# Optimization experiments

Measured on AMD Instinct MI355X. Metric: run time of the kernel, lower is better.

Reference implementation:

```python
import jax, jax.numpy as jnp
import numpy as np

B, N, T, D = 4, 128, 64, 768
L_ATTN, HEADS = 4, 8
M_SSM = 4
D_INNER, D_STATE, HEADDIM = 1536, 64, 64
NHEADS = D_INNER // HEADDIM  # 24
D_CONV = 4
CONV_DIM = D_INNER + 2 * D_STATE  # 1664
IN_PROJ = 2 * D_INNER + 2 * D_STATE + NHEADS  # 3224
FFN_MULT = 4


def rmsnorm(x, w, eps=1e-5):
    return x * jax.lax.rsqrt(jnp.mean(x * x, -1, keepdims=True) + eps) * w


def mha(q_in, kv_in, Wq, Wk, Wv, Wo):
    b, lq, d = q_in.shape
    lk = kv_in.shape[1]
    dh = d // HEADS
    scale = 1.0 / float(np.sqrt(dh))
    q = (q_in @ Wq).reshape(b, lq, HEADS, dh)
    k = (kv_in @ Wk).reshape(b, lk, HEADS, dh)
    v = (kv_in @ Wv).reshape(b, lk, HEADS, dh)
    scores = jnp.einsum('bqhd,bkhd->bhqk', q, k) * scale
    attn = jax.nn.softmax(scores, axis=-1)
    o = jnp.einsum('bhqk,bkhd->bqhd', attn, v).reshape(b, lq, d)
    return o @ Wo


def mamba_block(x, in_proj_w, conv_w, conv_b, dt_bias, A_log, D_skip, norm_w, out_proj_w):
    # x: (b, l, D); selective-scan (Mamba2) with scalar-per-head A, ngroups=1
    b, l, _ = x.shape
    zxbcdt = x @ in_proj_w                       # (b, l, IN_PROJ)
    z = zxbcdt[..., :D_INNER]
    xBC = zxbcdt[..., D_INNER:D_INNER + CONV_DIM]
    dt = zxbcdt[..., D_INNER + CONV_DIM:]        # (b, l, NHEADS)
    # causal depthwise conv1d, kernel D_CONV
    xp = jnp.pad(xBC, ((0, 0), (D_CONV - 1, 0), (0, 0)))
    xc = sum(conv_w[k] * xp[:, k:k + l] for k in range(D_CONV)) + conv_b
    xc = jax.nn.silu(xc)
    xs = xc[..., :D_INNER].reshape(b, l, NHEADS, HEADDIM)
    Bm = xc[..., D_INNER:D_INNER + D_STATE]      # (b, l, D_STATE)
    Cm = xc[..., D_INNER + D_STATE:]             # (b, l, D_STATE)
    dt = jax.nn.softplus(dt + dt_bias)           # (b, l, NHEADS)
    A = -jnp.exp(A_log)                          # (NHEADS,)
    h0 = jnp.zeros((b, NHEADS, HEADDIM, D_STATE), x.dtype)

    def step(h, inp):
        xt, Bt, Ct, dtt = inp                    # (b,nh,hd), (b,ds), (b,ds), (b,nh)
        dA = jnp.exp(dtt * A)                    # (b, nh)
        h = h * dA[:, :, None, None] + (dtt[:, :, None, None] * xt[..., None]) * Bt[:, None, None, :]
        y = jnp.einsum('bhps,bs->bhp', h, Ct)
        return h, y

    hT, ys = jax.lax.scan(step, h0, (xs.transpose(1, 0, 2, 3), Bm.transpose(1, 0, 2), Cm.transpose(1, 0, 2), dt.transpose(1, 0, 2)))
    y = ys.transpose(1, 0, 2, 3) + D_skip[:, None] * xs  # skip connection per head
    y = y.reshape(b, l, D_INNER)
    y = rmsnorm(y * jax.nn.silu(z), norm_w)      # gated RMSNorm
    return y @ out_proj_w, hT


def reference(precepts, actions, attn_norm1_w, Wq, Wk, Wv, Wo, attn_norm2_w, ffn_w1, ffn_b1, ffn_w2, ffn_b2, ssm_norm_w, in_proj_w, conv_w, conv_b, dt_bias, A_log, D_skip, mamba_norm_w, out_proj_w, proj_w, proj_b):
    p = precepts.reshape(B * N, T, D)
    a = actions.reshape(B * N, T, D)
    for i in range(L_ATTN):
        cross = (i + 1) % 2 == 0
        q = rmsnorm(p, attn_norm1_w[i])
        kv = a if cross else q
        p = p + mha(q, kv, Wq[i], Wk[i], Wv[i], Wo[i])
        h_ = rmsnorm(p, attn_norm2_w[i])
        p = p + (jax.nn.gelu(h_ @ ffn_w1[i] + ffn_b1[i]) @ ffn_w2[i] + ffn_b2[i])
    # (b n) t d -> (b t) n d : scan over the num_steps axis
    z = p.reshape(B, N, T, D).transpose(0, 2, 1, 3).reshape(B * T, N, D)
    h_last = None
    for m in range(M_SSM):
        out, h_last = mamba_block(rmsnorm(z, ssm_norm_w[m]), in_proj_w[m], conv_w[m], conv_b[m], dt_bias[m], A_log[m], D_skip[m], mamba_norm_w[m], out_proj_w[m])
        z = z + out
    y = z @ proj_w + proj_b
    y = y.reshape(B, T, N, D).transpose(0, 2, 1, 3)  # b n t d
    return y, h_last


def setup_inputs() -> dict:
    key = jax.random.key(0)
    ks = jax.random.split(key, 16)
    s = 0.02
    f32 = jnp.float32
    return {
        'precepts': jax.random.normal(ks[0], (B, N, T, D), f32),
        'actions': jax.random.normal(ks[1], (B, N, T, D), f32),
        'attn_norm1_w': jnp.ones((L_ATTN, D), f32),
        'Wq': s * jax.random.normal(ks[2], (L_ATTN, D, D), f32),
        'Wk': s * jax.random.normal(ks[3], (L_ATTN, D, D), f32),
        'Wv': s * jax.random.normal(ks[4], (L_ATTN, D, D), f32),
        'Wo': s * jax.random.normal(ks[5], (L_ATTN, D, D), f32),
        'attn_norm2_w': jnp.ones((L_ATTN, D), f32),
        'ffn_w1': s * jax.random.normal(ks[6], (L_ATTN, D, FFN_MULT * D), f32),
        'ffn_b1': jnp.zeros((L_ATTN, FFN_MULT * D), f32),
        'ffn_w2': s * jax.random.normal(ks[7], (L_ATTN, FFN_MULT * D, D), f32),
        'ffn_b2': jnp.zeros((L_ATTN, D), f32),
        'ssm_norm_w': jnp.ones((M_SSM, D), f32),
        'in_proj_w': s * jax.random.normal(ks[8], (M_SSM, D, IN_PROJ), f32),
        'conv_w': s * jax.random.normal(ks[9], (M_SSM, D_CONV, CONV_DIM), f32),
        'conv_b': jnp.zeros((M_SSM, CONV_DIM), f32),
        'dt_bias': jax.random.uniform(ks[10], (M_SSM, NHEADS), f32, -2.0, 0.0),
        'A_log': jnp.broadcast_to(jnp.log(jnp.arange(1, NHEADS + 1, dtype=f32)), (M_SSM, NHEADS)),
        'D_skip': jnp.ones((M_SSM, NHEADS), f32),
        'mamba_norm_w': jnp.ones((M_SSM, D_INNER), f32),
        'out_proj_w': s * jax.random.normal(ks[11], (M_SSM, D_INNER, D), f32),
        'proj_w': s * jax.random.normal(ks[12], (D, D), f32),
        'proj_b': jnp.zeros((D,), f32),
    }
```

## Files before the change

### kernel.cpp

```cpp
#include <hip/hip_runtime.h>
#include <hip/hip_bf16.h>
#include <math.h>

constexpr long TOK  = 32768;
constexpr long HALF = TOK * 768;
constexpr int FLAG_ACC = 1, FLAG_GELU = 2, FLAG_PERM = 4, FLAG_BF16 = 8;

typedef __bf16 bf16x8 __attribute__((ext_vector_type(8)));
typedef __bf16 bf16x4 __attribute__((ext_vector_type(4)));
typedef float  f32x4  __attribute__((ext_vector_type(4)));

__device__ __forceinline__ void gload_lds16(const void* g, void* l) {
    __builtin_amdgcn_global_load_lds(
        (const __attribute__((address_space(1))) void*)g,
        (__attribute__((address_space(3))) void*)l, 16, 0, 0);
}
__device__ __forceinline__ float bf2f(__hip_bfloat16 v) { return __bfloat162float(v); }

__global__ __launch_bounds__(256) void gemm_bf16(
    const __hip_bfloat16* __restrict__ A,
    const __hip_bfloat16* __restrict__ BT,
    const float* __restrict__ bias,
    void* __restrict__ Cv, int ldc,
    int M, int N, int K, int flags, int moff)
{
    __shared__ __hip_bfloat16 As[2][128 * 32];
    __shared__ __hip_bfloat16 Bs[2][128 * 32];
    const int tid = threadIdx.x;
    const int wv = tid >> 6, lane = tid & 63;
    const int nwg = gridDim.x * gridDim.y;
    const int orig = blockIdx.y * gridDim.x + blockIdx.x;
    const int q8 = nwg >> 3, r8 = nwg & 7;
    const int xcd = orig & 7, off = orig >> 3;
    const int wgid = (xcd < r8 ? xcd * (q8 + 1) : r8 * (q8 + 1) + (xcd - r8) * q8) + off;
    const int bm = (wgid / gridDim.x) * 128, bn = (wgid % gridDim.x) * 128;
    const int wr = (wv >> 1) * 64, wc = (wv & 1) * 64;
    const int lrow = lane & 15, lk = lane >> 4;
    const int ck = (lk ^ (lrow & 3) ^ ((lrow >> 2) & 3)) * 8;

    f32x4 acc[4][4];
#pragma unroll
    for (int n = 0; n < 4; n++)
#pragma unroll
        for (int m = 0; m < 4; m++) acc[n][m] = f32x4{0.f, 0.f, 0.f, 0.f};

    const int nk = K >> 5;
    auto stage = [&](int kt, int buf) {
#pragma unroll
        for (int i = 0; i < 2; i++) {
            const int lin = i * 256 + tid;
            const int row = lin >> 2;
            const int ks  = (((lin & 3) ^ (row & 3) ^ ((row >> 2) & 3)) * 8);
            const long asrc = (long)(bm + row) * K + kt * 32 + ks;
            const long bsrc = (long)(bn + row) * K + kt * 32 + ks;
            char* la = (char*)&As[buf][0] + (i * 256 + wv * 64) * 16;
            char* lb = (char*)&Bs[buf][0] + (i * 256 + wv * 64) * 16;
            gload_lds16(A + asrc, la);
            gload_lds16(BT + bsrc, lb);
        }
    };

    stage(0, 0);
    __syncthreads();
    for (int kt = 0; kt < nk; kt++) {
        const int cur = kt & 1;
        if (kt + 1 < nk) stage(kt + 1, cur ^ 1);
        bf16x8 af[4], bfr[4];
#pragma unroll
        for (int m = 0; m < 4; m++) {
            af[m]  = *(const bf16x8*)(const void*)&As[cur][(wr + m * 16 + lrow) * 32 + ck];
            bfr[m] = *(const bf16x8*)(const void*)&Bs[cur][(wc + m * 16 + lrow) * 32 + ck];
        }
#pragma unroll
        for (int n = 0; n < 4; n++)
#pragma unroll
            for (int m = 0; m < 4; m++)
                acc[n][m] = __builtin_amdgcn_mfma_f32_16x16x32_bf16(bfr[n], af[m], acc[n][m], 0, 0, 0);
        __syncthreads();
    }

    float* Cf = (float*)Cv;
    __hip_bfloat16* Cb = (__hip_bfloat16*)Cv;
#pragma unroll
    for (int n = 0; n < 4; n++) {
        const int gcb = bn + wc + n * 16 + lk * 4;
        f32x4 b4 = f32x4{0.f, 0.f, 0.f, 0.f};
        if (bias) b4 = *(const f32x4*)&bias[gcb];
#pragma unroll
        for (int m = 0; m < 4; m++) {
            const int gr = bm + wr + m * 16 + lrow;
            f32x4 v = acc[n][m] + b4;
            if (flags & FLAG_GELU) {
#pragma unroll
                for (int j = 0; j < 4; j++) {
                    const float x = v[j];
                    const float u = 1.5957691216057308f * (x + 0.044715f * x * x * x);
                    v[j] = x / (1.f + __expf(-u));
                }
            }
            if (flags & FLAG_PERM) {
                const int mg = moff + gr;
                const int b_ = mg >> 13, t_ = (mg >> 7) & 63, n_ = mg & 127;
                *(f32x4*)&Cf[(((long)(b_ * 128 + n_)) * 64 + t_) * ldc + gcb] = v;
            } else if (flags & FLAG_BF16) {
                __hip_bfloat16 o0 = __float2bfloat16(v[0]), o1 = __float2bfloat16(v[1]);
                __hip_bfloat16 o2 = __float2bfloat16(v[2]), o3 = __float2bfloat16(v[3]);
                ushort4 o = { *(ushort*)&o0, *(ushort*)&o1, *(ushort*)&o2, *(ushort*)&o3 };
                *(ushort4*)&Cb[(long)gr * ldc + gcb] = o;
            } else if (flags & FLAG_ACC) {
                float* dst = &Cf[(long)gr * ldc + gcb];
                f32x4 old = *(const f32x4*)dst;
                *(f32x4*)dst = old + v;
            } else {
                *(f32x4*)&Cf[(long)gr * ldc + gcb] = v;
            }
        }
    }
}

__global__ void convT_kernel(const float* __restrict__ W, __hip_bfloat16* __restrict__ WT,
                             int K, int N, int Npad)
{
    __shared__ float t[32][33];
    const int k0 = blockIdx.y * 32, n0 = blockIdx.x * 32;
    const int tx = threadIdx.x & 31, ty = threadIdx.x >> 5;
#pragma unroll
    for (int i = 0; i < 4; i++) {
        int k = k0 + ty + i * 8, n = n0 + tx;
        t[ty + i * 8][tx] = (k < K && n < N) ? W[(long)k * N + n] : 0.f;
    }
    __syncthreads();
#pragma unroll
    for (int i = 0; i < 4; i++) {
        int n = n0 + ty + i * 8, k = k0 + tx;
        if (n < Npad && k < K) WT[(long)n * K + k] = __float2bfloat16(t[tx][ty + i * 8]);
    }
}

__global__ void cvt_kernel(const float4* __restrict__ x, ushort4* __restrict__ y, long n4)
{
    long i = (long)blockIdx.x * 256 + threadIdx.x;
    if (i >= n4) return;
    float4 v = x[i];
    __hip_bfloat16 a = __float2bfloat16(v.x), b = __float2bfloat16(v.y);
    __hip_bfloat16 c = __float2bfloat16(v.z), d = __float2bfloat16(v.w);
    ushort4 o = { *(ushort*)&a, *(ushort*)&b, *(ushort*)&c, *(ushort*)&d };
    y[i] = o;
}

__global__ void rmsnorm_f32(const float* __restrict__ x, const float* __restrict__ w,
                            __hip_bfloat16* __restrict__ out, int D, int xs, int os, long nrows)
{
    const int wv = threadIdx.x >> 6, lane = threadIdx.x & 63;
    const long row = (long)blockIdx.x * 4 + wv;
    if (row >= nrows) return;
    const float* xr = x + row * xs;
    const int it = D >> 8;
    float ss = 0.f;
    for (int i = 0; i < it; i++) {
        const float4 v = *(const float4*)&xr[(i * 64 + lane) * 4];
        ss += v.x * v.x + v.y * v.y + v.z * v.z + v.w * v.w;
    }
    for (int o = 32; o; o >>= 1) ss += __shfl_xor(ss, o);
    const float sc = rsqrtf(ss / D + 1e-5f);
    __hip_bfloat16* orow = out + row * os;
    for (int i = 0; i < it; i++) {
        const int e = (i * 64 + lane) * 4;
        const float4 v = *(const float4*)&xr[e];
        const float4 g = *(const float4*)&w[e];
        bf16x4 o;
        o[0] = (__bf16)(v.x * sc * g.x); o[1] = (__bf16)(v.y * sc * g.y);
        o[2] = (__bf16)(v.z * sc * g.z); o[3] = (__bf16)(v.w * sc * g.w);
        *(bf16x4*)(void*)&orow[e] = o;
    }
}
__global__ void rmsnorm_b16(const __hip_bfloat16* __restrict__ x, const float* __restrict__ w,
                            __hip_bfloat16* __restrict__ out, int D, int xs, int os, long nrows)
{
    const int wv = threadIdx.x >> 6, lane = threadIdx.x & 63;
    const long row = (long)blockIdx.x * 4 + wv;
    if (row >= nrows) return;
    const __hip_bfloat16* xr = x + row * xs;
    const int it = D >> 8;
    float ss = 0.f;
    for (int i = 0; i < it; i++) {
        const bf16x4 v = *(const bf16x4*)(const void*)&xr[(i * 64 + lane) * 4];
#pragma unroll
        for (int e = 0; e < 4; e++) { const float f = (float)v[e]; ss += f * f; }
    }
    for (int o = 32; o; o >>= 1) ss += __shfl_xor(ss, o);
    const float sc = rsqrtf(ss / D + 1e-5f);
    __hip_bfloat16* orow = out + row * os;
    for (int i = 0; i < it; i++) {
        const int e = (i * 64 + lane) * 4;
        const bf16x4 v = *(const bf16x4*)(const void*)&xr[e];
        const float4 g = *(const float4*)&w[e];
        bf16x4 o;
        o[0] = (__bf16)((float)v[0] * sc * g.x); o[1] = (__bf16)((float)v[1] * sc * g.y);
        o[2] = (__bf16)((float)v[2] * sc * g.z); o[3] = (__bf16)((float)v[3] * sc * g.w);
        *(bf16x4*)(void*)&orow[e] = o;
    }
}

__global__ __launch_bounds__(256) void attn_kernel(
    const __hip_bfloat16* __restrict__ QKV, __hip_bfloat16* __restrict__ O)
{
    __shared__ __align__(16) __hip_bfloat16 Qs[3 * 64 * 32];
    __shared__ __align__(16) __hip_bfloat16 Ks[3 * 64 * 32];
    __shared__ __align__(16) __hip_bfloat16 VT[2 * 96 * 32];
    __shared__ __align__(16) __hip_bfloat16 Ps[2 * 64 * 32];
    const int tid = threadIdx.x;
    const int wid = tid >> 6, lane = tid & 63;
    const int lrow = lane & 15, lk = lane >> 4;
    const int b = blockIdx.x >> 3, h = blockIdx.x & 7;
    const long base = (long)b * 64 * 2304 + h * 96;

#pragma unroll
    for (int i = 0; i < 3; i++) {
        const int v = i * 256 + tid;
        const int r = v / 12, c8 = v - r * 12;
        const int kst = c8 >> 2, ch = c8 & 3, slot = ch ^ (r & 3);
        const bf16x8 q = *(const bf16x8*)(const void*)&QKV[base + (long)r * 2304 + c8 * 8];
        const bf16x8 k = *(const bf16x8*)(const void*)&QKV[base + (long)r * 2304 + 768 + c8 * 8];
        *(bf16x8*)(void*)&Qs[(kst * 64 + r) * 32 + slot * 8] = q;
        *(bf16x8*)(void*)&Ks[(kst * 64 + r) * 32 + slot * 8] = k;
    }
    for (int i = 0; i < 16; i++) {
        const int k = wid * 16 + i;
        const __hip_bfloat16* vrow = &QKV[base + (long)k * 2304 + 1536];
        const int sb = (k >> 3) & 3, khi = k >> 5, klo = k & 7;
        {
            const int d = lane;
            VT[(khi * 96 + d) * 32 + ((sb ^ (d & 3)) * 8) + klo] = vrow[d];
        }
        if (lane < 32) {
            const int d = 64 + lane;
            VT[(khi * 96 + d) * 32 + ((sb ^ (d & 3)) * 8) + klo] = vrow[d];
        }
    }
    __syncthreads();

    const int ck = (lk ^ (lrow & 3)) * 8;
    f32x4 s[4];
#pragma unroll
    for (int n = 0; n < 4; n++) s[n] = f32x4{0.f, 0.f, 0.f, 0.f};
#pragma unroll
    for (int kst = 0; kst < 3; kst++) {
        const bf16x8 qf = *(const bf16x8*)(const void*)&Qs[(kst * 64 + wid * 16 + lrow) * 32 + ck];
#pragma unroll
        for (int n = 0; n < 4; n++) {
            const bf16x8 kf = *(const bf16x8*)(const void*)&Ks[(kst * 64 + n * 16 + lrow) * 32 + ck];
            s[n] = __builtin_amdgcn_mfma_f32_16x16x32_bf16(qf, kf, s[n], 0, 0, 0);
        }
    }
    const float scale = 0.102062072615966f;
#pragma unroll
    for (int n = 0; n < 4; n++) s[n] *= scale;
    float inv[4];
#pragma unroll
    for (int j = 0; j < 4; j++) {
        float mx = fmaxf(fmaxf(s[0][j], s[1][j]), fmaxf(s[2][j], s[3][j]));
        mx = fmaxf(mx, __shfl_xor(mx, 1));
        mx = fmaxf(mx, __shfl_xor(mx, 2));
        mx = fmaxf(mx, __shfl_xor(mx, 4));
        mx = fmaxf(mx, __shfl_xor(mx, 8));
        float sum = 0.f;
#pragma unroll
        for (int n = 0; n < 4; n++) { s[n][j] = __expf(s[n][j] - mx); sum += s[n][j]; }
        sum += __shfl_xor(sum, 1);
        sum += __shfl_xor(sum, 2);
        sum += __shfl_xor(sum, 4);
        sum += __shfl_xor(sum, 8);
        inv[j] = 1.f / sum;
    }
#pragma unroll
    for (int n = 0; n < 4; n++) {
        const int k = n * 16 + lrow;
        const int kst = n >> 1, kc = ((n & 1) << 1) + (lrow >> 3), ke = lrow & 7;
#pragma unroll
        for (int j = 0; j < 4; j++) {
            const int q = wid * 16 + lk * 4 + j;
            Ps[(kst * 64 + q) * 32 + ((kc ^ (q & 3)) * 8) + ke] = __float2bfloat16(s[n][j] * inv[j]);
        }
    }
    __syncthreads();

    const int wq = wid >> 1, wd = wid & 1;
    f32x4 y[3][2];
#pragma unroll
    for (int mv = 0; mv < 3; mv++)
#pragma unroll
        for (int np = 0; np < 2; np++) y[mv][np] = f32x4{0.f, 0.f, 0.f, 0.f};
#pragma unroll
    for (int ks = 0; ks < 2; ks++) {
        bf16x8 vf[3], pf[2];
#pragma unroll
        for (int mv = 0; mv < 3; mv++)
            vf[mv] = *(const bf16x8*)(const void*)&VT[(ks * 96 + wd * 48 + mv * 16 + lrow) * 32 + ck];
#pragma unroll
        for (int np = 0; np < 2; np++)
            pf[np] = *(const bf16x8*)(const void*)&Ps[(ks * 64 + wq * 32 + np * 16 + lrow) * 32 + ck];
#pragma unroll
        for (int mv = 0; mv < 3; mv++)
#pragma unroll
            for (int np = 0; np < 2; np++)
                y[mv][np] = __builtin_amdgcn_mfma_f32_16x16x32_bf16(vf[mv], pf[np], y[mv][np], 0, 0, 0);
    }
#pragma unroll
    for (int mv = 0; mv < 3; mv++) {
        const int d0 = wd * 48 + mv * 16 + lk * 4;
#pragma unroll
        for (int np = 0; np < 2; np++) {
            const int q = wq * 32 + np * 16 + lrow;
            bf16x4 o;
#pragma unroll
            for (int j = 0; j < 4; j++) o[j] = (__bf16)y[mv][np][j];
            *(bf16x4*)(void*)&O[(long)(b * 64 + q) * 768 + h * 96 + d0] = o;
        }
    }
}

__global__ void transpose_kernel(const float* __restrict__ P, float* __restrict__ Z)
{
    long lin = (long)blockIdx.x * 256 + threadIdx.x;
    if (lin >= HALF) return;
    int d = (int)(lin % 768);
    long rowz = lin / 768;
    int n = rowz & 127, t = (int)((rowz >> 7) & 63), b = (int)(rowz >> 13);
    long rowp = ((long)(b * 128 + n)) * 64 + t;
    Z[lin] = P[rowp * 768 + d];
}

__global__ __launch_bounds__(256) void conv_kernel(
    const __hip_bfloat16* __restrict__ zx, const float* __restrict__ cw,
    const float* __restrict__ cb, __hip_bfloat16* __restrict__ xc,
    __hip_bfloat16* __restrict__ bcB, long rows)
{
    const long r = blockIdx.x;
    const int tid = threadIdx.x;
    if (tid >= 208) return;
    const int c0 = tid * 8;
    const int n = (int)(r & 127);
    float acc[8];
    {
        const float4 b0 = *(const float4*)&cb[c0];
        const float4 b1 = *(const float4*)&cb[c0 + 4];
        acc[0] = b0.x; acc[1] = b0.y; acc[2] = b0.z; acc[3] = b0.w;
        acc[4] = b1.x; acc[5] = b1.y; acc[6] = b1.z; acc[7] = b1.w;
    }
#pragma unroll
    for (int k = 0; k < 4; k++) {
        if (n - 3 + k < 0) continue;
        const bf16x8 xv = *(const bf16x8*)(const void*)&zx[(r - 3 + k) * 3328 + 1536 + c0];
        const float4 w0 = *(const float4*)&cw[k * 1664 + c0];
        const float4 w1 = *(const float4*)&cw[k * 1664 + c0 + 4];
        acc[0] += w0.x * (float)xv[0]; acc[1] += w0.y * (float)xv[1];
        acc[2] += w0.z * (float)xv[2]; acc[3] += w0.w * (float)xv[3];
        acc[4] += w1.x * (float)xv[4]; acc[5] += w1.y * (float)xv[5];
        acc[6] += w1.z * (float)xv[6]; acc[7] += w1.w * (float)xv[7];
    }
    bf16x8 o;
#pragma unroll
    for (int e = 0; e < 8; e++) {
        const float s = acc[e] / (1.f + __expf(-acc[e]));
        o[e] = (__bf16)s;
    }
    if (c0 < 1536) *(bf16x8*)(void*)&xc[r * 1664 + c0] = o;
    else           *(bf16x8*)(void*)&bcB[r * 128 + (c0 - 1536)] = o;
}

__global__ void dt_kernel(const __hip_bfloat16* __restrict__ zx, const float* __restrict__ bias,
                          float* __restrict__ dtf, long count)
{
    long lin = (long)blockIdx.x * 256 + threadIdx.x;
    if (lin >= count) return;
    int h = (int)(lin % 24);
    long r = lin / 24;
    float v = bf2f(zx[r * 3328 + 3200 + h]) + bias[h];
    dtf[lin] = (v > 0.f) ? v + log1pf(expf(-v)) : log1pf(expf(v));
}

__global__ __launch_bounds__(256) void ssd_kernel(
    const __hip_bfloat16* __restrict__ zx0, const float* __restrict__ dtf0,
    const __hip_bfloat16* __restrict__ bcB0, __hip_bfloat16* __restrict__ xc0,
    const float* __restrict__ Alog, const float* __restrict__ Dskip,
    float* __restrict__ hout, int bt0)
{
    __shared__ __align__(16) char SM[50688];
    __hip_bfloat16* Cl  = (__hip_bfloat16*)SM;
    __hip_bfloat16* Bl  = Cl + 8192;
    __hip_bfloat16* Ml  = (__hip_bfloat16*)SM;
    __hip_bfloat16* XTl = (__hip_bfloat16*)(SM + 32768);
    __hip_bfloat16* BTl = (__hip_bfloat16*)SM;
    float* cum = (float*)(SM + 49152);
    float* dtl = cum + 128;
    float* wl  = dtl + 128;

    const int tid = threadIdx.x;
    const int wid = tid >> 6, lane = tid & 63;
    const int lrow = lane & 15, lk = lane >> 4;
    const int btl = blockIdx.x / 24, h = blockIdx.x % 24;
    const long rowbase = (long)btl * 128;

    const __hip_bfloat16* zxp = zx0 + rowbase * 3328 + h * 64;
    const float* dtp = dtf0 + rowbase * 24;
    const __hip_bfloat16* bcp = bcB0 + rowbase * 128;
    __hip_bfloat16* xcp = xc0 + rowbase * 1664 + h * 64;

    const float A  = -expf(Alog[h]);
    const float Dh = Dskip[h];

#pragma unroll
    for (int i = 0; i < 4; i++) {
        const int v = tid + i * 256;
        const int row = v >> 3, c8 = v & 7;
        const int kst = c8 >> 2, ch = c8 & 3;
        const int slot = ch ^ (row & 3);
        bf16x8 vB = *(const bf16x8*)(const void*)&bcp[(long)row * 128 + c8 * 8];
        bf16x8 vC = *(const bf16x8*)(const void*)&bcp[(long)row * 128 + 64 + c8 * 8];
        *(bf16x8*)(void*)&Bl[(kst * 128 + row) * 32 + slot * 8] = vB;
        *(bf16x8*)(void*)&Cl[(kst * 128 + row) * 32 + slot * 8] = vC;
    }
    for (int i = 0; i < 32; i++) {
        const int t = wid * 32 + i;
        const int slot = (i >> 3) ^ (lane & 3);
        XTl[(wid * 64 + lane) * 32 + slot * 8 + (i & 7)] = xcp[(long)t * 1664 + lane];
    }
    if (tid < 128) dtl[tid] = dtp[(long)tid * 24 + h];
    __syncthreads();
    if (tid < 128) cum[tid] = dtl[tid] * A;
    __syncthreads();
    for (int off = 1; off < 128; off <<= 1) {
        float v = 0.f;
        if (tid < 128 && tid >= off) v = cum[tid - off];
        __syncthreads();
        if (tid < 128) cum[tid] += v;
        __syncthreads();
    }
    if (tid < 128) wl[tid] = expf(cum[127] - cum[tid]) * dtl[tid];
    __syncthreads();

    const int wr1 = (wid >> 1) * 64, wc1 = (wid & 1) * 64;
    const int ck = (lk ^ (lrow & 3)) * 8;
    f32x4 a1[4][4];
#pragma unroll
    for (int m = 0; m < 4; m++)
#pragma unroll
        for (int n = 0; n < 4; n++) a1[m][n] = f32x4{0.f, 0.f, 0.f, 0.f};
#pragma unroll
    for (int kst = 0; kst < 2; kst++) {
        bf16x8 ca[4], bb[4];
#pragma unroll
        for (int m = 0; m < 4; m++)
            ca[m] = *(const bf16x8*)(const void*)&Cl[(kst * 128 + wr1 + m * 16 + lrow) * 32 + ck];
#pragma unroll
        for (int n = 0; n < 4; n++)
            bb[n] = *(const bf16x8*)(const void*)&Bl[(kst * 128 + wc1 + n * 16 + lrow) * 32 + ck];
#pragma unroll
        for (int m = 0; m < 4; m++)
#pragma unroll
            for (int n = 0; n < 4; n++)
                a1[m][n] = __builtin_amdgcn_mfma_f32_16x16x32_bf16(ca[m], bb[n], a1[m][n], 0, 0, 0);
    }
    __syncthreads();

#pragma unroll
    for (int m = 0; m < 4; m++) {
        const int tb = wr1 + m * 16 + lk * 4;
        const f32x4 c4 = *(const f32x4*)&cum[tb];
#pragma unroll
        for (int n = 0; n < 4; n++) {
            const int j = wc1 + n * 16 + lrow;
            const float cj = cum[j], dj = dtl[j];
            const int jst = j >> 5, jc = (j >> 3) & 3, je = j & 7;
#pragma unroll
            for (int jj = 0; jj < 4; jj++) {
                const int t = tb + jj;
                float val = 0.f;
                if (j <= t) val = a1[m][n][jj] * expf(c4[jj] - cj) * dj;
                Ml[(jst * 128 + t) * 32 + ((jc ^ (t & 3)) * 8) + je] = __float2bfloat16(val);
            }
        }
    }
    __syncthreads();

    const int wr2 = (wid >> 1) * 64, wc2 = (wid & 1) * 32;
    f32x4 a2[4][2];
#pragma unroll
    for (int m = 0; m < 4; m++)
#pragma unroll
        for (int n = 0; n < 2; n++) a2[m][n] = f32x4{0.f, 0.f, 0.f, 0.f};
#pragma unroll
    for (int kst = 0; kst < 4; kst++) {
        bf16x8 am[4], bn[2];
#pragma unroll
        for (int m = 0; m < 4; m++)
            am[m] = *(const bf16x8*)(const void*)&Ml[(kst * 128 + wr2 + m * 16 + lrow) * 32 + ck];
#pragma unroll
        for (int n = 0; n < 2; n++)
            bn[n] = *(const bf16x8*)(const void*)&XTl[(kst * 64 + wc2 + n * 16 + lrow) * 32 + ck];
#pragma unroll
        for (int m = 0; m < 4; m++)
#pragma unroll
            for (int n = 0; n < 2; n++)
                a2[m][n] = __builtin_amdgcn_mfma_f32_16x16x32_bf16(am[m], bn[n], a2[m][n], 0, 0, 0);
    }

#pragma unroll
    for (int m = 0; m < 4; m++) {
        const int tb = wr2 + m * 16 + lk * 4;
#pragma unroll
        for (int n = 0; n < 2; n++) {
            const int p = wc2 + n * 16 + lrow;
#pragma unroll
            for (int jj = 0; jj < 4; jj++) {
                const int t = tb + jj;
                const float x = bf2f(XTl[((t >> 5) * 64 + p) * 32 + ((((t >> 3) & 3) ^ (p & 3)) * 8) + (t & 7)]);
                const float zg = bf2f(zxp[(long)t * 3328 + p]);
                const float y = (a2[m][n][jj] + Dh * x) * (zg / (1.f + expf(-zg)));
                xcp[(long)t * 1664 + p] = __float2bfloat16(y);
            }
        }
    }

    if (hout) {
        __syncthreads();
        for (int i = 0; i < 32; i++) {
            const int j = wid * 32 + i;
            const int slot = (i >> 3) ^ (lane & 3);
            BTl[(wid * 64 + lane) * 32 + slot * 8 + (j & 7)] = bcp[(long)j * 128 + lane];
        }
        __syncthreads();
        const int wrp = (wid >> 1) * 32, wcs = (wid & 1) * 32;
        f32x4 a3[2][2];
#pragma unroll
        for (int m = 0; m < 2; m++)
#pragma unroll
            for (int n = 0; n < 2; n++) a3[m][n] = f32x4{0.f, 0.f, 0.f, 0.f};
#pragma unroll
        for (int kst = 0; kst < 4; kst++) {
            const int jb = kst * 32 + lk * 8;
            const f32x4 wa = *(const f32x4*)&wl[jb];
            const f32x4 wb = *(const f32x4*)&wl[jb + 4];
            bf16x8 xw[2], bn[2];
#pragma unroll
            for (int m = 0; m < 2; m++) {
                bf16x8 xr = *(const bf16x8*)(const void*)&XTl[(kst * 64 + wrp + m * 16 + lrow) * 32 + ck];
                bf16x8 t;
#pragma unroll
                for (int e = 0; e < 4; e++) t[e] = (__bf16)((float)xr[e] * wa[e]);
#pragma unroll
                for (int e = 0; e < 4; e++) t[4 + e] = (__bf16)((float)xr[4 + e] * wb[e]);
                xw[m] = t;
            }
#pragma unroll
            for (int n = 0; n < 2; n++)
                bn[n] = *(const bf16x8*)(const void*)&BTl[(kst * 64 + wcs + n * 16 + lrow) * 32 + ck];
#pragma unroll
            for (int m = 0; m < 2; m++)
#pragma unroll
                for (int n = 0; n < 2; n++)
                    a3[m][n] = __builtin_amdgcn_mfma_f32_16x16x32_bf16(xw[m], bn[n], a3[m][n], 0, 0, 0);
        }
        float* hp = hout + ((long)(bt0 + btl) * 24 + h) * 4096;
#pragma unroll
        for (int m = 0; m < 2; m++) {
            const int pb = wrp + m * 16 + lk * 4;
#pragma unroll
            for (int n = 0; n < 2; n++) {
                const int s = wcs + n * 16 + lrow;
#pragma unroll
                for (int jj = 0; jj < 4; jj++)
                    hp[(long)(pb + jj) * 64 + s] = a3[m][n][jj];
            }
        }
    }
}

extern "C" void kernel_launch(void* const* d_in, const int* in_sizes, int n_in,
                              void* d_out, int out_size, void* d_ws, size_t ws_size,
                              hipStream_t stream)
{
    const float* precepts  = (const float*)d_in[0];
    const float* actions   = (const float*)d_in[1];
    const float* attn_n1   = (const float*)d_in[2];
    const float* Wq        = (const float*)d_in[3];
    const float* Wk        = (const float*)d_in[4];
    const float* Wv        = (const float*)d_in[5];
    const float* Wo        = (const float*)d_in[6];
    const float* attn_n2   = (const float*)d_in[7];
    const float* ffn_w1    = (const float*)d_in[8];
    const float* ffn_b1    = (const float*)d_in[9];
    const float* ffn_w2    = (const float*)d_in[10];
    const float* ffn_b2    = (const float*)d_in[11];
    const float* ssm_norm  = (const float*)d_in[12];
    const float* in_proj   = (const float*)d_in[13];
    const float* conv_w    = (const float*)d_in[14];
    const float* conv_b    = (const float*)d_in[15];
    const float* dt_bias   = (const float*)d_in[16];
    const float* A_log     = (const float*)d_in[17];
    const float* D_skip    = (const float*)d_in[18];
    const float* mamba_nw  = (const float*)d_in[19];
    const float* out_proj  = (const float*)d_in[20];
    const float* proj_w    = (const float*)d_in[21];
    const float* proj_b    = (const float*)d_in[22];

    float* out  = (float*)d_out;
    float* Z    = out;
    float* P    = out + HALF;
    float* hout = out + HALF;

    __hip_bfloat16* wb = (__hip_bfloat16*)d_ws;
    long wo = 0;
    auto walloc = [&](long els) { __hip_bfloat16* p = wb + wo; wo += els; return p; };
    __hip_bfloat16* WqkvT = walloc(4L * 2304 * 768);
    __hip_bfloat16* W1T   = walloc(4L * 3072 * 768);
    __hip_bfloat16* W2T   = walloc(4L * 768 * 3072);
    __hip_bfloat16* inT   = walloc(4L * 3328 * 768);
    __hip_bfloat16* outT  = walloc(4L * 768 * 1536);
    __hip_bfloat16* projT = walloc(768L * 768);
    __hip_bfloat16* WoT   = walloc(4L * 768 * 768);
    char* pbase = (char*)(wb + ((wo + 255) & ~255L));
    const size_t used_w = (size_t)(pbase - (char*)d_ws);
    const size_t avail = ws_size > used_w ? ws_size - used_w : 0;

    int CB = 512;
    while (CB > 8 && (unsigned long long)CB * 884736ull > avail) CB >>= 1;
    int CBT = 256;
    while (CBT > 2 && (unsigned long long)CBT * 1912832ull > avail) CBT >>= 1;

    auto gemm = [&](const __hip_bfloat16* A, const __hip_bfloat16* BT, const float* bias,
                    void* C, int ldc, int M, int N, int Npad, int K, int flags, int moff) {
        dim3 g(Npad / 128, M / 128);
        hipLaunchKernelGGL(gemm_bf16, g, dim3(256), 0, stream,
                           A, BT, bias, C, ldc, M, N, K, flags, moff);
    };
    auto cvtT = [&](const float* W, __hip_bfloat16* WT, int K, int N, int Npad) {
        dim3 g((Npad + 31) / 32, (K + 31) / 32);
        hipLaunchKernelGGL(convT_kernel, g, dim3(256), 0, stream, W, WT, K, N, Npad);
    };
    auto cvt = [&](const float* x, __hip_bfloat16* y, long n) {
        long n4 = n / 4;
        hipLaunchKernelGGL(cvt_kernel, dim3((n4 + 255) / 256), dim3(256), 0, stream,
                           (const float4*)x, (ushort4*)y, n4);
    };
    auto rmsF = [&](const float* x, const float* w, __hip_bfloat16* o, int D, int xs, int os, long rows) {
        hipLaunchKernelGGL(rmsnorm_f32, dim3((rows + 3) / 4), dim3(256), 0, stream,
                           x, w, o, D, xs, os, rows);
    };
    auto rmsB = [&](const __hip_bfloat16* x, const float* w, __hip_bfloat16* o, int D, int xs, int os, long rows) {
        hipLaunchKernelGGL(rmsnorm_b16, dim3((rows + 3) / 4), dim3(256), 0, stream,
                           x, w, o, D, xs, os, rows);
    };

    for (int l = 0; l < 4; l++) {
        cvtT(Wq + (long)l * 589824, WqkvT + (long)l * 2304 * 768,                768, 768, 768);
        cvtT(Wk + (long)l * 589824, WqkvT + (long)l * 2304 * 768 +  768L * 768,  768, 768, 768);
        cvtT(Wv + (long)l * 589824, WqkvT + (long)l * 2304 * 768 + 1536L * 768,  768, 768, 768);
        cvtT(Wo + (long)l * 589824, WoT + (long)l * 589824, 768, 768, 768);
        cvtT(ffn_w1 + (long)l * 2359296, W1T + (long)l * 2359296, 768, 3072, 3072);
        cvtT(ffn_w2 + (long)l * 2359296, W2T + (long)l * 2359296, 3072, 768, 768);
    }
    for (int m = 0; m < 4; m++) {
        cvtT(in_proj + (long)m * 768 * 3224, inT + (long)m * 3328 * 768, 768, 3224, 3328);
        cvtT(out_proj + (long)m * 1536 * 768, outT + (long)m * 768 * 1536, 1536, 768, 768);
    }
    cvtT(proj_w, projT, 768, 768, 768);

    hipMemcpyAsync(P, precepts, HALF * sizeof(float), hipMemcpyDeviceToDevice, stream);
    {
        const long rA = (long)CB * 64;
        __hip_bfloat16* bufA   = (__hip_bfloat16*)pbase;
        __hip_bfloat16* actB   = bufA + rA * 768;
        __hip_bfloat16* bufQKV = actB + rA * 768;
        __hip_bfloat16* bufH   = bufQKV + rA * 2304;
        const int nac = 512 / CB;
        const int Mr = (int)rA;
        if (nac == 1) cvt(actions, actB, rA * 768);
        for (int layer = 0; layer < 4; layer++) {
            const bool cross = ((layer + 1) % 2) == 0;
            for (int c = 0; c < nac; c++) {
                const long tok0 = (long)c * rA;
                float* Pc = P + tok0 * 768;
                rmsF(Pc, attn_n1 + layer * 768, bufA, 768, 768, 768, Mr);
                if (!cross) {
                    gemm(bufA, WqkvT + (long)layer * 2304 * 768, nullptr, bufQKV, 2304,
                         Mr, 2304, 2304, 768, FLAG_BF16, 0);
                } else {
                    if (nac != 1) cvt(actions + tok0 * 768, actB, rA * 768);
                    gemm(bufA, WqkvT + (long)layer * 2304 * 768, nullptr, bufQKV, 2304,
                         Mr, 768, 768, 768, FLAG_BF16, 0);
                    gemm(actB, WqkvT + (long)layer * 2304 * 768 + 768L * 768, nullptr,
                         bufQKV + 768, 2304, Mr, 1536, 1536, 768, FLAG_BF16, 0);
                }
                hipLaunchKernelGGL(attn_kernel, dim3(CB * 8), dim3(256), 0, stream,
                                   bufQKV, bufA);
                gemm(bufA, WoT + (long)layer * 589824, nullptr, Pc, 768,
                     Mr, 768, 768, 768, FLAG_ACC, 0);
                rmsF(Pc, attn_n2 + layer * 768, bufA, 768, 768, 768, Mr);
                gemm(bufA, W1T + (long)layer * 2359296, ffn_b1 + layer * 3072, bufH, 3072,
                     Mr, 3072, 3072, 768, FLAG_GELU | FLAG_BF16, 0);
                gemm(bufH, W2T + (long)layer * 2359296, ffn_b2 + layer * 768, Pc, 768,
                     Mr, 768, 768, 3072, FLAG_ACC, 0);
            }
        }
    }

    hipLaunchKernelGGL(transpose_kernel, dim3((int)((HALF + 255) / 256)), dim3(256), 0, stream, P, Z);

    {
        const long rM = (long)CBT * 128;
        __hip_bfloat16* xn  = (__hip_bfloat16*)pbase;
        __hip_bfloat16* zx  = xn + rM * 768;
        float*          dtf = (float*)(zx + rM * 3328);
        __hip_bfloat16* xc  = (__hip_bfloat16*)(dtf + rM * 24);
        __hip_bfloat16* yb  = xc + rM * 1664;
        __hip_bfloat16* bcB = yb + rM * 1536;
        const int nmc = 256 / CBT;
        const int Mr = (int)rM;
        for (int m = 0; m < 4; m++) {
            for (int c = 0; c < nmc; c++) {
                float* Zc = Z + (long)c * rM * 768;
                rmsF(Zc, ssm_norm + m * 768, xn, 768, 768, 768, Mr);
                gemm(xn, inT + (long)m * 3328 * 768, nullptr, zx, 3328,
                     Mr, 3224, 3328, 768, FLAG_BF16, 0);
                hipLaunchKernelGGL(conv_kernel, dim3((int)rM), dim3(256), 0, stream,
                                   zx, conv_w + m * 4 * 1664, conv_b + m * 1664, xc, bcB, rM);
                const long dtn = rM * 24;
                hipLaunchKernelGGL(dt_kernel, dim3((int)((dtn + 255) / 256)), dim3(256), 0, stream,
                                   zx, dt_bias + m * 24, dtf, dtn);
                hipLaunchKernelGGL(ssd_kernel, dim3(CBT * 24), dim3(256), 0, stream,
                                   zx, dtf, bcB, xc, A_log + m * 24, D_skip + m * 24,
                                   (m == 3) ? hout : nullptr, c * CBT);
                rmsB(xc, mamba_nw + m * 1536, yb, 1536, 1664, 1536, Mr);
                gemm(yb, outT + (long)m * 768 * 1536, nullptr, Zc, 768,
                     Mr, 768, 768, 1536, FLAG_ACC, 0);
            }
        }
    }

    {
        __hip_bfloat16* Zb = (__hip_bfloat16*)pbase;
        cvt(Z, Zb, HALF);
        gemm(Zb, projT, proj_b, out, 768, 32768, 768, 768, 768, FLAG_PERM, 0);
    }
}
```

Before: 7.090 ms.

## Add 256x256 bf16 MFMA GEMM kernel with swizzled LDS and staged prefetch

Adds a new 512-thread GEMM with 256x256 output tiles and K-step 64. It uses XOR-swizzled LDS layouts, direct global-to-LDS loads issued in four quarter-stages interleaved with MFMA phases, and s_setprio around the compute blocks. The dispatcher uses it whenever M and Npad are multiples of 256, and otherwise falls back to the old 128x128 kernel. Larger tiles raise data reuse per LDS load and cut global traffic, at the cost of 128KB of LDS, more registers, and fewer workgroups for the smaller GEMMs. A column bound check for N is also added to the epilogues.

```diff
diff --git a/kernel.cpp b/kernel.cpp
--- a/kernel.cpp
+++ b/kernel.cpp
@@ -16,6 +16,186 @@
         (__attribute__((address_space(3))) void*)l, 16, 0, 0);
 }
 __device__ __forceinline__ float bf2f(__hip_bfloat16 v) { return __bfloat162float(v); }
+
+__global__ __launch_bounds__(512, 2) void gemm256(
+    const __hip_bfloat16* __restrict__ A,
+    const __hip_bfloat16* __restrict__ BT,
+    const float* __restrict__ bias,
+    void* __restrict__ Cv, int ldc,
+    int M, int N, int K, int flags, int moff)
+{
+    __shared__ __hip_bfloat16 As[2][256 * 64];
+    __shared__ __hip_bfloat16 Bs[2][256 * 64];
+    const int tid = threadIdx.x;
+    const int wid = tid >> 6, lane = tid & 63;
+    const int wm = wid >> 2, wn = wid & 3;
+    const int lrow = lane & 15, lk = lane >> 4;
+    const int nwg = gridDim.x * gridDim.y;
+    const int orig = blockIdx.y * gridDim.x + blockIdx.x;
+    const int q8 = nwg >> 3, r8 = nwg & 7;
+    const int xcd = orig & 7, off = orig >> 3;
+    const int wgid = (xcd < r8 ? xcd * (q8 + 1) : r8 * (q8 + 1) + (xcd - r8) * q8) + off;
+    const int bm = (wgid / gridDim.x) * 256, bn = (wgid % gridDim.x) * 256;
+    const int nk = K >> 6;
+
+    f32x4 acc[4][8];
+#pragma unroll
+    for (int nf = 0; nf < 4; nf++)
+#pragma unroll
+        for (int mf = 0; mf < 8; mf++) acc[nf][mf] = f32x4{0.f, 0.f, 0.f, 0.f};
+
+    bf16x8 Af[4][2];
+    bf16x8 B0[2][2];
+    bf16x8 B1[2][2];
+
+    auto stage = [&](int kt, int which) {
+        if (kt >= nk) return;
+        const int dbuf = kt & 1;
+        __hip_bfloat16* lbase = (which >= 2 ? &Bs[dbuf][0] : &As[dbuf][0]) + (which & 1) * 8192;
+        const __hip_bfloat16* g = (which >= 2 ? BT : A);
+        const int trow = (which >= 2 ? bn : bm) + (which & 1) * 128;
+#pragma unroll
+        for (int i = 0; i < 2; i++) {
+            const int slot = i * 512 + tid;
+            const int rl = slot >> 3, ch = slot & 7;
+            const int sc = (ch ^ (rl & 7)) * 8;
+            const long src = (long)(trow + rl) * K + (long)kt * 64 + sc;
+            char* l = (char*)lbase + (i * 512 + wid * 64) * 16;
+            gload_lds16(g + src, l);
+        }
+    };
+    auto readA = [&](int dbuf, int mh) {
+#pragma unroll
+        for (int mq = 0; mq < 4; mq++)
+#pragma unroll
+            for (int ks = 0; ks < 2; ks++) {
+                const int r = wm * 128 + mh * 64 + mq * 16 + lrow;
+                const int ch = ((ks * 4 + lk) ^ (r & 7)) * 8;
+                Af[mq][ks] = *(const bf16x8*)(const void*)&As[dbuf][r * 64 + ch];
+            }
+    };
+    auto readB0 = [&](int dbuf) {
+#pragma unroll
+        for (int nf = 0; nf < 2; nf++)
+#pragma unroll
+            for (int ks = 0; ks < 2; ks++) {
+                const int r = wn * 64 + nf * 16 + lrow;
+                const int ch = ((ks * 4 + lk) ^ (r & 7)) * 8;
+                B0[nf][ks] = *(const bf16x8*)(const void*)&Bs[dbuf][r * 64 + ch];
+            }
+    };
+    auto readB1 = [&](int dbuf) {
+#pragma unroll
+        for (int nf = 0; nf < 2; nf++)
+#pragma unroll
+            for (int ks = 0; ks < 2; ks++) {
+                const int r = wn * 64 + (2 + nf) * 16 + lrow;
+                const int ch = ((ks * 4 + lk) ^ (r & 7)) * 8;
+                B1[nf][ks] = *(const bf16x8*)(const void*)&Bs[dbuf][r * 64 + ch];
+            }
+    };
+
+    stage(0, 0); stage(0, 1); stage(0, 2); stage(0, 3);
+    stage(1, 2); stage(1, 3);
+    asm volatile("s_waitcnt vmcnt(4)" ::: "memory");
+    __builtin_amdgcn_s_barrier();
+
+    for (int kt = 0; kt < nk; kt++) {
+        const int cur = kt & 1;
+        readA(cur, 0); readB0(cur);
+        stage(kt + 1, 0);
+        __builtin_amdgcn_s_barrier();
+        __builtin_amdgcn_s_setprio(1);
+#pragma unroll
+        for (int nf = 0; nf < 2; nf++)
+#pragma unroll
+            for (int mq = 0; mq < 4; mq++)
+#pragma unroll
+                for (int ks = 0; ks < 2; ks++)
+                    acc[nf][mq] = __builtin_amdgcn_mfma_f32_16x16x32_bf16(B0[nf][ks], Af[mq][ks], acc[nf][mq], 0, 0, 0);
+        __builtin_amdgcn_s_setprio(0);
+        __builtin_amdgcn_s_barrier();
+        readB1(cur);
+        stage(kt + 1, 1);
+        __builtin_amdgcn_s_barrier();
+        __builtin_amdgcn_s_setprio(1);
+#pragma unroll
+        for (int nf = 0; nf < 2; nf++)
+#pragma unroll
+            for (int mq = 0; mq < 4; mq++)
+#pragma unroll
+                for (int ks = 0; ks < 2; ks++)
+                    acc[2 + nf][mq] = __builtin_amdgcn_mfma_f32_16x16x32_bf16(B1[nf][ks], Af[mq][ks], acc[2 + nf][mq], 0, 0, 0);
+        __builtin_amdgcn_s_setprio(0);
+        __builtin_amdgcn_s_barrier();
+        readA(cur, 1);
+        stage(kt + 2, 2);
+        __builtin_amdgcn_s_barrier();
+        __builtin_amdgcn_s_setprio(1);
+#pragma unroll
+        for (int nf = 0; nf < 2; nf++)
+#pragma unroll
+            for (int mq = 0; mq < 4; mq++)
+#pragma unroll
+                for (int ks = 0; ks < 2; ks++)
+                    acc[2 + nf][4 + mq] = __builtin_amdgcn_mfma_f32_16x16x32_bf16(B1[nf][ks], Af[mq][ks], acc[2 + nf][4 + mq], 0, 0, 0);
+        __builtin_amdgcn_s_setprio(0);
+        __builtin_amdgcn_s_barrier();
+        stage(kt + 2, 3);
+        if (kt + 2 < nk) asm volatile("s_waitcnt vmcnt(4)" ::: "memory");
+        else             asm volatile("s_waitcnt vmcnt(0)" ::: "memory");
+        __builtin_amdgcn_s_barrier();
+        __builtin_amdgcn_s_setprio(1);
+#pragma unroll
+        for (int nf = 0; nf < 2; nf++)
+#pragma unroll
+            for (int mq = 0; mq < 4; mq++)
+#pragma unroll
+                for (int ks = 0; ks < 2; ks++)
+                    acc[nf][4 + mq] = __builtin_amdgcn_mfma_f32_16x16x32_bf16(B0[nf][ks], Af[mq][ks], acc[nf][4 + mq], 0, 0, 0);
+        __builtin_amdgcn_s_setprio(0);
+        __builtin_amdgcn_s_barrier();
+    }
+
+    float* Cf = (float*)Cv;
+    __hip_bfloat16* Cb = (__hip_bfloat16*)Cv;
+#pragma unroll
+    for (int nf = 0; nf < 4; nf++) {
+        const int gcb = bn + wn * 64 + nf * 16 + lk * 4;
+        if (gcb >= N) continue;
+        f32x4 b4 = f32x4{0.f, 0.f, 0.f, 0.f};
+        if (bias) b4 = *(const f32x4*)&bias[gcb];
+#pragma unroll
+        for (int mf = 0; mf < 8; mf++) {
+            const int gr = bm + wm * 128 + mf * 16 + lrow;
+            f32x4 v = acc[nf][mf] + b4;
+            if (flags & FLAG_GELU) {
+#pragma unroll
+                for (int j = 0; j < 4; j++) {
+                    const float x = v[j];
+                    const float u = 1.5957691216057308f * (x + 0.044715f * x * x * x);
+                    v[j] = x / (1.f + __expf(-u));
+                }
+            }
+            if (flags & FLAG_PERM) {
+                const int mg = moff + gr;
+                const int b_ = mg >> 13, t_ = (mg >> 7) & 63, n_ = mg & 127;
+                *(f32x4*)&Cf[(((long)(b_ * 128 + n_)) * 64 + t_) * ldc + gcb] = v;
+            } else if (flags & FLAG_BF16) {
+                __hip_bfloat16 o0 = __float2bfloat16(v[0]), o1 = __float2bfloat16(v[1]);
+                __hip_bfloat16 o2 = __float2bfloat16(v[2]), o3 = __float2bfloat16(v[3]);
+                ushort4 o = { *(ushort*)&o0, *(ushort*)&o1, *(ushort*)&o2, *(ushort*)&o3 };
+                *(ushort4*)&Cb[(long)gr * ldc + gcb] = o;
+            } else if (flags & FLAG_ACC) {
+                float* dst = &Cf[(long)gr * ldc + gcb];
+                f32x4 old = *(const f32x4*)dst;
+                *(f32x4*)dst = old + v;
+            } else {
+                *(f32x4*)&Cf[(long)gr * ldc + gcb] = v;
+            }
+        }
+    }
+}
 
 __global__ __launch_bounds__(256) void gemm_bf16(
     const __hip_bfloat16* __restrict__ A,
@@ -84,6 +264,7 @@
 #pragma unroll
     for (int n = 0; n < 4; n++) {
         const int gcb = bn + wc + n * 16 + lk * 4;
+        if (gcb >= N) continue;
         f32x4 b4 = f32x4{0.f, 0.f, 0.f, 0.f};
         if (bias) b4 = *(const f32x4*)&bias[gcb];
 #pragma unroll
@@ -631,9 +812,15 @@
 
     auto gemm = [&](const __hip_bfloat16* A, const __hip_bfloat16* BT, const float* bias,
                     void* C, int ldc, int M, int N, int Npad, int K, int flags, int moff) {
-        dim3 g(Npad / 128, M / 128);
-        hipLaunchKernelGGL(gemm_bf16, g, dim3(256), 0, stream,
-                           A, BT, bias, C, ldc, M, N, K, flags, moff);
+        if ((M & 255) == 0 && (Npad & 255) == 0 && (K & 63) == 0) {
+            dim3 g(Npad / 256, M / 256);
+            hipLaunchKernelGGL(gemm256, g, dim3(512), 0, stream,
+                               A, BT, bias, C, ldc, M, N, K, flags, moff);
+        } else {
+            dim3 g(Npad / 128, M / 128);
+            hipLaunchKernelGGL(gemm_bf16, g, dim3(256), 0, stream,
+                               A, BT, bias, C, ldc, M, N, K, flags, moff);
+        }
     };
     auto cvtT = [&](const float* W, __hip_bfloat16* WT, int K, int N, int Npad) {
         dim3 g((Npad + 31) / 32, (K + 31) / 32);
```

New measurement: 7.152 ms. No clear change (+0.9%).
